# Kernel optimization log

Measured on AMD Instinct MI355X. Metric: run time of the kernel, lower is better.

The kernel has to match this reference:

```python
import jax, jax.numpy as jnp
import numpy as np

N_ATOM_TYPES = 100
EMBED_DIM = 32
HIDDEN_DIM = 256
B, W, D = 16, 256, 64


def setup_inputs() -> dict:
    key = jax.random.key(0)
    ks = jax.random.split(key, 16)
    inp = {
        "atom1_idx": jax.random.randint(ks[0], (B, W, D), 0, N_ATOM_TYPES),
        "atom2_idx": jax.random.randint(ks[1], (B, W, D), 0, N_ATOM_TYPES),
        "distances": jax.random.uniform(ks[2], (B, W, D), jnp.float32) * 20.0,
        "mask": jax.random.bernoulli(ks[3], 0.9, (B, W, D)),
        # parameters
        "atom_embed": jax.random.normal(ks[4], (N_ATOM_TYPES + 1, EMBED_DIM), jnp.float32) * 0.02,
        "w_in": jax.random.normal(ks[5], (2 * EMBED_DIM + 1, HIDDEN_DIM), jnp.float32) * 0.05,
        "b_in": jnp.zeros((HIDDEN_DIM,), jnp.float32),
        "w_a1": jax.random.normal(ks[6], (HIDDEN_DIM, HIDDEN_DIM // 4), jnp.float32) * 0.05,
        "b_a1": jnp.zeros((HIDDEN_DIM // 4,), jnp.float32),
        "w_a2": jax.random.normal(ks[7], (HIDDEN_DIM // 4, 1), jnp.float32) * 0.05,
        "b_a2": jnp.zeros((1,), jnp.float32),
        "w_v1": jax.random.normal(ks[8], (HIDDEN_DIM, HIDDEN_DIM), jnp.float32) * 0.05,
        "b_v1": jnp.zeros((HIDDEN_DIM,), jnp.float32),
        "w_v2": jax.random.normal(ks[9], (HIDDEN_DIM, HIDDEN_DIM), jnp.float32) * 0.05,
        "b_v2": jnp.zeros((HIDDEN_DIM,), jnp.float32),
        "fallback": jnp.zeros((HIDDEN_DIM,), jnp.float32),
    }
    return inp


def _gelu(x):
    return jax.nn.gelu(x, approximate=False)  # torch default GELU is exact erf form


def reference(atom1_idx, atom2_idx, distances, mask,
              atom_embed, w_in, b_in, w_a1, b_a1, w_a2, b_a2,
              w_v1, b_v1, w_v2, b_v2, fallback):
    # zero padding row (padding_idx = n_atom_types); also kills its grad like torch
    pad = atom_embed.shape[0] - 1
    table = atom_embed * (jnp.arange(atom_embed.shape[0]) != pad)[:, None]
    e1 = table[atom1_idx]                     # [B,W,D,E]
    e2 = table[atom2_idx]                     # [B,W,D,E]
    d = distances * mask.astype(distances.dtype)
    combined = jnp.concatenate([e1, e2, d[..., None]], axis=-1)   # [B,W,D,2E+1]
    hidden = _gelu(combined @ w_in + b_in)    # [B,W,D,H] (dropout = identity in eval)
    scores = (_gelu(hidden @ w_a1 + b_a1) @ w_a2 + b_a2)[..., 0]  # [B,W,D]
    scores = jnp.where(mask, scores, jnp.float32(-10000.0))
    attn = jax.nn.softmax(scores, axis=-1)    # [B,W,D]
    values = _gelu(hidden @ w_v1 + b_v1) @ w_v2 + b_v2            # [B,W,D,H]
    out = jnp.sum(values * attn[..., None], axis=2)               # [B,W,H]
    any_valid = jnp.any(mask, axis=2)
    return jnp.where(any_valid[..., None], out, fallback)
```

## Files before the change

kernel.cpp:

```cpp
#include <hip/hip_runtime.h>
#include <math.h>

#define BW 4096
#define DD 64
#define HH 256

typedef __bf16 bf16x8 __attribute__((ext_vector_type(8)));
typedef float  f32x4  __attribute__((ext_vector_type(4)));
typedef unsigned short u16x8 __attribute__((ext_vector_type(8)));

#define WIN_OFF 0
#define WA1_OFF 16384
#define WV1_OFF 32768
#define WV2_OFF 98304

__device__ __forceinline__ unsigned short to_bf16u(float f) {
    union { __bf16 b; unsigned short u; } cv;
    cv.b = (__bf16)f;
    return cv.u;
}

__device__ __forceinline__ float gelu_fast(float x) {
    float x2 = x * x;
    float z  = x * __builtin_fmaf(-0.10294344f, x2, -2.3022082f);
    float e  = __builtin_amdgcn_exp2f(z);
    return x * __builtin_amdgcn_rcpf(1.0f + e);
}

__device__ __forceinline__ f32x4 mfma16(bf16x8 a, bf16x8 b, f32x4 c) {
    return __builtin_amdgcn_mfma_f32_16x16x32_bf16(a, b, c, 0, 0, 0);
}

__global__ void pack_weights(const float* __restrict__ w_in,
                             const float* __restrict__ w_a1,
                             const float* __restrict__ w_v1,
                             const float* __restrict__ w_v2,
                             unsigned short* __restrict__ ws) {
    int t = blockIdx.x * 256 + threadIdx.x;
    if (t >= 20480) return;
    int lane = t & 63;
    int g = lane >> 4, li = lane & 15;
    u16x8 v;
    if (t < 2048) {
        int fr = t >> 6;
        int kin = fr >> 4, ht = fr & 15;
        #pragma unroll
        for (int j = 0; j < 8; ++j) {
            int k = kin * 32 + 8 * g + j;
            v[j] = to_bf16u(w_in[(size_t)k * 256 + 16 * ht + li]);
        }
        *(u16x8*)(ws + WIN_OFF + (size_t)t * 8) = v;
    } else if (t < 4096) {
        int c = t - 2048;
        int fr = c >> 6;
        int kt = fr >> 2, ct = fr & 3;
        #pragma unroll
        for (int j = 0; j < 8; ++j) {
            int k = kt * 32 + 16 * (j >> 2) + 4 * g + (j & 3);
            v[j] = to_bf16u(w_a1[(size_t)k * 64 + ct * 16 + li]);
        }
        *(u16x8*)(ws + WA1_OFF + (size_t)c * 8) = v;
    } else if (t < 12288) {
        int c = t - 4096;
        int fr = c >> 6;
        int kt = fr >> 4, ct = fr & 15;
        #pragma unroll
        for (int j = 0; j < 8; ++j) {
            int k = kt * 32 + 16 * (j >> 2) + 4 * g + (j & 3);
            v[j] = to_bf16u(w_v1[(size_t)k * 256 + ct * 16 + li]);
        }
        *(u16x8*)(ws + WV1_OFF + (size_t)c * 8) = v;
    } else {
        int c = t - 12288;
        int fr = c >> 6;
        int kt = fr >> 4, ct = fr & 15;
        #pragma unroll
        for (int j = 0; j < 8; ++j) {
            int k = kt * 32 + 8 * g + j;
            v[j] = to_bf16u(w_v2[(size_t)k * 256 + ct * 16 + li]);
        }
        *(u16x8*)(ws + WV2_OFF + (size_t)c * 8) = v;
    }
}

__global__ __launch_bounds__(256, 4)
void dist_attn_kernel(const int*   __restrict__ a1,
                      const int*   __restrict__ a2,
                      const float* __restrict__ dist,
                      const int*   __restrict__ mask,
                      const float* __restrict__ table,
                      const float* __restrict__ w_in,
                      const float* __restrict__ b_in,
                      const float* __restrict__ b_a1,
                      const float* __restrict__ w_a2,
                      const float* __restrict__ b_a2,
                      const float* __restrict__ b_v1,
                      const float* __restrict__ b_v2,
                      const float* __restrict__ fb,
                      const unsigned short* __restrict__ ws,
                      float*       __restrict__ out) {
    __shared__ __align__(16) unsigned short hidfrag[4][8][64][8];
    __shared__ __align__(16) float scorep[256];
    __shared__ __align__(16) float attn_s[256];
    __shared__ __align__(16) unsigned short r_bf[256];

    const int tid = threadIdx.x;
    const int l   = tid & 63;
    const int w   = tid >> 6;
    const int g   = l >> 4;
    const int li  = l & 15;
    const int blk = blockIdx.x;
    const long base = (long)blk * DD;

    {
        bf16x8 cb[4][2];
        float  dmv[4];
        #pragma unroll
        for (int dt = 0; dt < 4; ++dt) {
            const int i1 = a1[base + 16 * dt + li];
            const int i2 = a2[base + 16 * dt + li];
            const int m  = mask[base + 16 * dt + li];
            dmv[dt] = m ? dist[base + 16 * dt + li] : 0.0f;
            const float* s1 = table + (size_t)i1 * 32 + 8 * g;
            const float* s2 = table + (size_t)i2 * 32 + 8 * g;
            f32x4 v0 = *(const f32x4*)s1;
            f32x4 v1 = *(const f32x4*)(s1 + 4);
            f32x4 v2 = *(const f32x4*)s2;
            f32x4 v3 = *(const f32x4*)(s2 + 4);
            #pragma unroll
            for (int j = 0; j < 4; ++j) {
                cb[dt][0][j]     = (__bf16)v0[j];
                cb[dt][0][j + 4] = (__bf16)v1[j];
                cb[dt][1][j]     = (__bf16)v2[j];
                cb[dt][1][j + 4] = (__bf16)v3[j];
            }
        }
        #pragma unroll
        for (int hp = 0; hp < 2; ++hp) {
            bf16x8 pend[4];
            #pragma unroll
            for (int b = 0; b < 2; ++b) {
                const int ht = 4 * w + 2 * hp + b;
                bf16x8 af0 = *(const bf16x8*)(ws + WIN_OFF + ((size_t)(0 * 16 + ht) * 64 + l) * 8);
                bf16x8 af1 = *(const bf16x8*)(ws + WIN_OFF + ((size_t)(1 * 16 + ht) * 64 + l) * 8);
                f32x4 w64v = *(const f32x4*)&w_in[64 * 256 + 16 * ht + 4 * g];
                f32x4 binv = *(const f32x4*)&b_in[16 * ht + 4 * g];
                #pragma unroll
                for (int dt = 0; dt < 4; ++dt) {
                    f32x4 acc;
                    #pragma unroll
                    for (int p = 0; p < 4; ++p)
                        acc[p] = __builtin_fmaf(dmv[dt], w64v[p], binv[p]);
                    acc = mfma16(af0, cb[dt][0], acc);
                    acc = mfma16(af1, cb[dt][1], acc);
                    #pragma unroll
                    for (int p = 0; p < 4; ++p)
                        pend[dt][4 * b + p] = (__bf16)gelu_fast(acc[p]);
                }
            }
            #pragma unroll
            for (int dt = 0; dt < 4; ++dt)
                *(bf16x8*)&hidfrag[dt][2 * w + hp][l][0] = pend[dt];
        }
    }
    __syncthreads();

    {
        bf16x8 ba[8];
        #pragma unroll
        for (int kt = 0; kt < 8; ++kt)
            ba[kt] = *(const bf16x8*)(ws + WA1_OFF + ((size_t)(kt * 4 + w) * 64 + l) * 8);
        f32x4 acc2[4];
        #pragma unroll
        for (int rt = 0; rt < 4; ++rt) acc2[rt] = (f32x4){0.f, 0.f, 0.f, 0.f};
        #pragma unroll
        for (int kt = 0; kt < 8; ++kt) {
            #pragma unroll
            for (int rt = 0; rt < 4; ++rt) {
                bf16x8 a = *(const bf16x8*)&hidfrag[rt][kt][l][0];
                acc2[rt] = mfma16(a, ba[kt], acc2[rt]);
            }
        }
        const float ba1 = b_a1[16 * w + li];
        const float wa2 = w_a2[16 * w + li];
        #pragma unroll
        for (int rt = 0; rt < 4; ++rt) {
            float s[4];
            #pragma unroll
            for (int p = 0; p < 4; ++p) s[p] = gelu_fast(acc2[rt][p] + ba1) * wa2;
            #pragma unroll
            for (int off = 1; off <= 8; off <<= 1)
                #pragma unroll
                for (int p = 0; p < 4; ++p) s[p] += __shfl_xor(s[p], off, 64);
            if (li == 0) {
                f32x4 sv; sv[0] = s[0]; sv[1] = s[1]; sv[2] = s[2]; sv[3] = s[3];
                *(f32x4*)&scorep[w * 64 + 16 * rt + 4 * g] = sv;
            }
        }
    }
    __syncthreads();

    {
        const int m = mask[base + l];
        float sc = scorep[l] + scorep[64 + l] + scorep[128 + l] + scorep[192 + l] + b_a2[0];
        if (!m) sc = -10000.0f;
        float mx = sc;
        #pragma unroll
        for (int off = 32; off; off >>= 1) mx = fmaxf(mx, __shfl_xor(mx, off, 64));
        float p = __expf(sc - mx);
        float sm = p;
        #pragma unroll
        for (int off = 32; off; off >>= 1) sm += __shfl_xor(sm, off, 64);
        attn_s[w * 64 + l] = p / sm;
    }

    {
        f32x4 av[4];
        #pragma unroll
        for (int rt = 0; rt < 4; ++rt) av[rt] = *(const f32x4*)&attn_s[w * 64 + 16 * rt + 4 * g];
        #pragma unroll
        for (int half = 0; half < 2; ++half) {
            f32x4 acc3[2][4];
            #pragma unroll
            for (int c2 = 0; c2 < 2; ++c2)
                #pragma unroll
                for (int rt = 0; rt < 4; ++rt) acc3[c2][rt] = (f32x4){0.f, 0.f, 0.f, 0.f};
            #pragma unroll
            for (int kt = 0; kt < 8; ++kt) {
                bf16x8 b0 = *(const bf16x8*)(ws + WV1_OFF + ((size_t)(kt * 16 + 4 * w + 2 * half + 0) * 64 + l) * 8);
                bf16x8 b1 = *(const bf16x8*)(ws + WV1_OFF + ((size_t)(kt * 16 + 4 * w + 2 * half + 1) * 64 + l) * 8);
                bf16x8 a[4];
                #pragma unroll
                for (int rt = 0; rt < 4; ++rt) a[rt] = *(const bf16x8*)&hidfrag[rt][kt][l][0];
                #pragma unroll
                for (int rt = 0; rt < 4; ++rt) {
                    acc3[0][rt] = mfma16(a[rt], b0, acc3[0][rt]);
                    acc3[1][rt] = mfma16(a[rt], b1, acc3[1][rt]);
                }
            }
            #pragma unroll
            for (int c2 = 0; c2 < 2; ++c2) {
                const int ct = 2 * half + c2;
                const int c = 64 * w + 16 * ct + li;
                const float bv = b_v1[c];
                float val = 0.f;
                #pragma unroll
                for (int rt = 0; rt < 4; ++rt)
                    #pragma unroll
                    for (int p = 0; p < 4; ++p)
                        val += av[rt][p] * gelu_fast(acc3[c2][rt][p] + bv);
                val += __shfl_xor(val, 16, 64);
                val += __shfl_xor(val, 32, 64);
                if (g == 0) r_bf[c] = to_bf16u(val);
            }
        }
    }
    __syncthreads();

    {
        const int anyv = __any(mask[base + l] != 0);
        f32x4 acc[4];
        #pragma unroll
        for (int ct = 0; ct < 4; ++ct) acc[ct] = (f32x4){0.f, 0.f, 0.f, 0.f};
        #pragma unroll
        for (int kt = 0; kt < 8; ++kt) {
            bf16x8 a = *(const bf16x8*)&r_bf[kt * 32 + 8 * g];
            #pragma unroll
            for (int ct = 0; ct < 4; ++ct) {
                bf16x8 b = *(const bf16x8*)(ws + WV2_OFF + ((size_t)(kt * 16 + 4 * w + ct) * 64 + l) * 8);
                acc[ct] = mfma16(a, b, acc[ct]);
            }
        }
        if (g == 0) {
            #pragma unroll
            for (int ct = 0; ct < 4; ++ct) {
                const int c = 16 * (4 * w + ct) + li;
                float o = acc[ct][0] + b_v2[c];
                if (!anyv) o = fb[c];
                out[(size_t)blk * HH + c] = o;
            }
        }
    }
}

extern "C" void kernel_launch(void* const* d_in, const int* in_sizes, int n_in,
                              void* d_out, int out_size, void* d_ws, size_t ws_size,
                              hipStream_t stream) {
    const int*   a1    = (const int*)  d_in[0];
    const int*   a2    = (const int*)  d_in[1];
    const float* dist  = (const float*)d_in[2];
    const int*   mask  = (const int*)  d_in[3];
    const float* table = (const float*)d_in[4];
    const float* w_in  = (const float*)d_in[5];
    const float* b_in  = (const float*)d_in[6];
    const float* w_a1  = (const float*)d_in[7];
    const float* b_a1  = (const float*)d_in[8];
    const float* w_a2  = (const float*)d_in[9];
    const float* b_a2  = (const float*)d_in[10];
    const float* w_v1  = (const float*)d_in[11];
    const float* b_v1  = (const float*)d_in[12];
    const float* w_v2  = (const float*)d_in[13];
    const float* b_v2  = (const float*)d_in[14];
    const float* fb    = (const float*)d_in[15];
    float* out = (float*)d_out;
    unsigned short* ws = (unsigned short*)d_ws;

    pack_weights<<<80, 256, 0, stream>>>(w_in, w_a1, w_v1, w_v2, ws);
    dist_attn_kernel<<<BW, 256, 0, stream>>>(a1, a2, dist, mask, table,
                                             w_in, b_in, b_a1, w_a2, b_a2,
                                             b_v1, b_v2, fb, ws, out);
}
```

Measured before the change: 111.2 us.

## Use single-wavefront blocks with hidden activations kept in registers

```diff
diff --git a/kernel.cpp b/kernel.cpp
--- a/kernel.cpp
+++ b/kernel.cpp
@@ -83,7 +83,7 @@
     }
 }
 
-__global__ __launch_bounds__(256, 4)
+__global__ __launch_bounds__(64, 2)
 void dist_attn_kernel(const int*   __restrict__ a1,
                       const int*   __restrict__ a2,
                       const float* __restrict__ dist,
@@ -99,19 +99,18 @@
                       const float* __restrict__ fb,
                       const unsigned short* __restrict__ ws,
                       float*       __restrict__ out) {
-    __shared__ __align__(16) unsigned short hidfrag[4][8][64][8];
-    __shared__ __align__(16) float scorep[256];
-    __shared__ __align__(16) float attn_s[256];
-    __shared__ __align__(16) unsigned short r_bf[256];
-
-    const int tid = threadIdx.x;
-    const int l   = tid & 63;
-    const int w   = tid >> 6;
-    const int g   = l >> 4;
-    const int li  = l & 15;
-    const int blk = blockIdx.x;
-    const long base = (long)blk * DD;
-
+    __shared__ float          score_s[64];
+    __shared__ float          attn_sh[64];
+    __shared__ unsigned short r_bf[256];
+
+    const int l  = threadIdx.x;
+    const int g  = l >> 4;
+    const int li = l & 15;
+    const long base = (long)blockIdx.x * DD;
+
+    bf16x8 hidA[4][8];
+
+    int mvec[4];
     {
         bf16x8 cb[4][2];
         float  dmv[4];
@@ -120,6 +119,7 @@
             const int i1 = a1[base + 16 * dt + li];
             const int i2 = a2[base + 16 * dt + li];
             const int m  = mask[base + 16 * dt + li];
+            mvec[dt] = m;
             dmv[dt] = m ? dist[base + 16 * dt + li] : 0.0f;
             const float* s1 = table + (size_t)i1 * 32 + 8 * g;
             const float* s2 = table + (size_t)i2 * 32 + 8 * g;
@@ -136,11 +136,11 @@
             }
         }
         #pragma unroll
-        for (int hp = 0; hp < 2; ++hp) {
+        for (int kt = 0; kt < 8; ++kt) {
             bf16x8 pend[4];
             #pragma unroll
             for (int b = 0; b < 2; ++b) {
-                const int ht = 4 * w + 2 * hp + b;
+                const int ht = 2 * kt + b;
                 bf16x8 af0 = *(const bf16x8*)(ws + WIN_OFF + ((size_t)(0 * 16 + ht) * 64 + l) * 8);
                 bf16x8 af1 = *(const bf16x8*)(ws + WIN_OFF + ((size_t)(1 * 16 + ht) * 64 + l) * 8);
                 f32x4 w64v = *(const f32x4*)&w_in[64 * 256 + 16 * ht + 4 * g];
@@ -160,49 +160,53 @@
             }
             #pragma unroll
             for (int dt = 0; dt < 4; ++dt)
-                *(bf16x8*)&hidfrag[dt][2 * w + hp][l][0] = pend[dt];
-        }
-    }
-    __syncthreads();
-
-    {
-        bf16x8 ba[8];
-        #pragma unroll
-        for (int kt = 0; kt < 8; ++kt)
-            ba[kt] = *(const bf16x8*)(ws + WA1_OFF + ((size_t)(kt * 4 + w) * 64 + l) * 8);
-        f32x4 acc2[4];
-        #pragma unroll
-        for (int rt = 0; rt < 4; ++rt) acc2[rt] = (f32x4){0.f, 0.f, 0.f, 0.f};
-        #pragma unroll
-        for (int kt = 0; kt < 8; ++kt) {
+                hidA[dt][kt] = pend[dt];
+        }
+    }
+
+    {
+        f32x4 spart[4];
+        #pragma unroll
+        for (int rt = 0; rt < 4; ++rt) spart[rt] = (f32x4){0.f, 0.f, 0.f, 0.f};
+        #pragma unroll
+        for (int ct = 0; ct < 4; ++ct) {
+            f32x4 acc2[4];
+            #pragma unroll
+            for (int rt = 0; rt < 4; ++rt) acc2[rt] = (f32x4){0.f, 0.f, 0.f, 0.f};
+            #pragma unroll
+            for (int kt = 0; kt < 8; ++kt) {
+                bf16x8 bfr = *(const bf16x8*)(ws + WA1_OFF + ((size_t)(kt * 4 + ct) * 64 + l) * 8);
+                #pragma unroll
+                for (int rt = 0; rt < 4; ++rt)
+                    acc2[rt] = mfma16(hidA[rt][kt], bfr, acc2[rt]);
+            }
+            const float ba1 = b_a1[16 * ct + li];
+            const float wa2 = w_a2[16 * ct + li];
             #pragma unroll
             for (int rt = 0; rt < 4; ++rt) {
-                bf16x8 a = *(const bf16x8*)&hidfrag[rt][kt][l][0];
-                acc2[rt] = mfma16(a, ba[kt], acc2[rt]);
-            }
-        }
-        const float ba1 = b_a1[16 * w + li];
-        const float wa2 = w_a2[16 * w + li];
-        #pragma unroll
-        for (int rt = 0; rt < 4; ++rt) {
-            float s[4];
-            #pragma unroll
-            for (int p = 0; p < 4; ++p) s[p] = gelu_fast(acc2[rt][p] + ba1) * wa2;
-            #pragma unroll
-            for (int off = 1; off <= 8; off <<= 1)
-                #pragma unroll
-                for (int p = 0; p < 4; ++p) s[p] += __shfl_xor(s[p], off, 64);
-            if (li == 0) {
-                f32x4 sv; sv[0] = s[0]; sv[1] = s[1]; sv[2] = s[2]; sv[3] = s[3];
-                *(f32x4*)&scorep[w * 64 + 16 * rt + 4 * g] = sv;
-            }
-        }
-    }
-    __syncthreads();
-
+                float s[4];
+                #pragma unroll
+                for (int p = 0; p < 4; ++p) s[p] = gelu_fast(acc2[rt][p] + ba1) * wa2;
+                #pragma unroll
+                for (int off = 1; off <= 8; off <<= 1)
+                    #pragma unroll
+                    for (int p = 0; p < 4; ++p) s[p] += __shfl_xor(s[p], off, 64);
+                #pragma unroll
+                for (int p = 0; p < 4; ++p) spart[rt][p] += s[p];
+            }
+        }
+        if (li == 0) {
+            #pragma unroll
+            for (int rt = 0; rt < 4; ++rt)
+                *(f32x4*)&score_s[16 * rt + 4 * g] = spart[rt];
+        }
+    }
+
+    int anyv;
     {
         const int m = mask[base + l];
-        float sc = scorep[l] + scorep[64 + l] + scorep[128 + l] + scorep[192 + l] + b_a2[0];
+        anyv = __any(m != 0);
+        float sc = score_s[l] + b_a2[0];
         if (!m) sc = -10000.0f;
         float mx = sc;
         #pragma unroll
@@ -211,15 +215,15 @@
         float sm = p;
         #pragma unroll
         for (int off = 32; off; off >>= 1) sm += __shfl_xor(sm, off, 64);
-        attn_s[w * 64 + l] = p / sm;
+        attn_sh[l] = p / sm;
     }
 
     {
         f32x4 av[4];
         #pragma unroll
-        for (int rt = 0; rt < 4; ++rt) av[rt] = *(const f32x4*)&attn_s[w * 64 + 16 * rt + 4 * g];
-        #pragma unroll
-        for (int half = 0; half < 2; ++half) {
+        for (int rt = 0; rt < 4; ++rt) av[rt] = *(const f32x4*)&attn_sh[16 * rt + 4 * g];
+        #pragma unroll
+        for (int cp = 0; cp < 8; ++cp) {
             f32x4 acc3[2][4];
             #pragma unroll
             for (int c2 = 0; c2 < 2; ++c2)
@@ -227,21 +231,17 @@
                 for (int rt = 0; rt < 4; ++rt) acc3[c2][rt] = (f32x4){0.f, 0.f, 0.f, 0.f};
             #pragma unroll
             for (int kt = 0; kt < 8; ++kt) {
-                bf16x8 b0 = *(const bf16x8*)(ws + WV1_OFF + ((size_t)(kt * 16 + 4 * w + 2 * half + 0) * 64 + l) * 8);
-                bf16x8 b1 = *(const bf16x8*)(ws + WV1_OFF + ((size_t)(kt * 16 + 4 * w + 2 * half + 1) * 64 + l) * 8);
-                bf16x8 a[4];
-                #pragma unroll
-                for (int rt = 0; rt < 4; ++rt) a[rt] = *(const bf16x8*)&hidfrag[rt][kt][l][0];
+                bf16x8 b0 = *(const bf16x8*)(ws + WV1_OFF + ((size_t)(kt * 16 + 2 * cp + 0) * 64 + l) * 8);
+                bf16x8 b1 = *(const bf16x8*)(ws + WV1_OFF + ((size_t)(kt * 16 + 2 * cp + 1) * 64 + l) * 8);
                 #pragma unroll
                 for (int rt = 0; rt < 4; ++rt) {
-                    acc3[0][rt] = mfma16(a[rt], b0, acc3[0][rt]);
-                    acc3[1][rt] = mfma16(a[rt], b1, acc3[1][rt]);
+                    acc3[0][rt] = mfma16(hidA[rt][kt], b0, acc3[0][rt]);
+                    acc3[1][rt] = mfma16(hidA[rt][kt], b1, acc3[1][rt]);
                 }
             }
             #pragma unroll
             for (int c2 = 0; c2 < 2; ++c2) {
-                const int ct = 2 * half + c2;
-                const int c = 64 * w + 16 * ct + li;
+                const int c = 16 * (2 * cp + c2) + li;
                 const float bv = b_v1[c];
                 float val = 0.f;
                 #pragma unroll
@@ -255,29 +255,30 @@
             }
         }
     }
-    __syncthreads();
-
-    {
-        const int anyv = __any(mask[base + l] != 0);
-        f32x4 acc[4];
-        #pragma unroll
-        for (int ct = 0; ct < 4; ++ct) acc[ct] = (f32x4){0.f, 0.f, 0.f, 0.f};
-        #pragma unroll
-        for (int kt = 0; kt < 8; ++kt) {
-            bf16x8 a = *(const bf16x8*)&r_bf[kt * 32 + 8 * g];
-            #pragma unroll
-            for (int ct = 0; ct < 4; ++ct) {
-                bf16x8 b = *(const bf16x8*)(ws + WV2_OFF + ((size_t)(kt * 16 + 4 * w + ct) * 64 + l) * 8);
-                acc[ct] = mfma16(a, b, acc[ct]);
-            }
-        }
-        if (g == 0) {
-            #pragma unroll
-            for (int ct = 0; ct < 4; ++ct) {
-                const int c = 16 * (4 * w + ct) + li;
-                float o = acc[ct][0] + b_v2[c];
-                if (!anyv) o = fb[c];
-                out[(size_t)blk * HH + c] = o;
+
+    {
+        #pragma unroll
+        for (int q = 0; q < 4; ++q) {
+            f32x4 acc[4];
+            #pragma unroll
+            for (int c4 = 0; c4 < 4; ++c4) acc[c4] = (f32x4){0.f, 0.f, 0.f, 0.f};
+            #pragma unroll
+            for (int kt = 0; kt < 8; ++kt) {
+                bf16x8 a = *(const bf16x8*)&r_bf[kt * 32 + 8 * g];
+                #pragma unroll
+                for (int c4 = 0; c4 < 4; ++c4) {
+                    bf16x8 b = *(const bf16x8*)(ws + WV2_OFF + ((size_t)(kt * 16 + 4 * q + c4) * 64 + l) * 8);
+                    acc[c4] = mfma16(a, b, acc[c4]);
+                }
+            }
+            if (g == 0) {
+                #pragma unroll
+                for (int c4 = 0; c4 < 4; ++c4) {
+                    const int c = 16 * (4 * q + c4) + li;
+                    float o = acc[c4][0] + b_v2[c];
+                    if (!anyv) o = fb[c];
+                    out[(size_t)blockIdx.x * HH + c] = o;
+                }
             }
         }
     }
@@ -306,7 +307,7 @@
     unsigned short* ws = (unsigned short*)d_ws;
 
     pack_weights<<<80, 256, 0, stream>>>(w_in, w_a1, w_v1, w_v2, ws);
-    dist_attn_kernel<<<BW, 256, 0, stream>>>(a1, a2, dist, mask, table,
-                                             w_in, b_in, b_a1, w_a2, b_a2,
-                                             b_v1, b_v2, fb, ws, out);
-}
+    dist_attn_kernel<<<BW, 64, 0, stream>>>(a1, a2, dist, mask, table,
+                                            w_in, b_in, b_a1, w_a2, b_a2,
+                                            b_v1, b_v2, fb, ws, out);
+}
```

After: 107.0 us. -3.8%, faster.
